# Optimization experiments

Hardware: AMD Instinct MI355X
Metric: run time of the kernel (lower is better)

The kernel has to match this reference:

```python
import jax, jax.numpy as jnp
import numpy as np

B = 16384        # batch
N_IN = 784       # n_input_neurons
D = 64           # n_neurons_per_hidd_bank
N_LAYERS = 6     # layers of hidden banks
BANKS = 6        # banks per layer (n_hidd_banks = 36)
N_OUT = 10       # n_output_neurons
EPS = 1e-5       # BatchNorm1d eps


def setup_inputs() -> dict:
    key = jax.random.key(0)
    ks = jax.random.split(key, 8)
    x = jax.random.normal(ks[0], (B, N_IN), dtype=jnp.float32)
    gamma_in = jnp.ones((N_IN,), jnp.float32)
    beta_in = jnp.zeros((N_IN,), jnp.float32)
    # input2hidden Linear(N_IN -> D) for each of the 6 input banks (layer 0)
    W_in = jax.random.normal(ks[1], (BANKS, D, N_IN), jnp.float32) * 0.03
    b_in = jax.random.normal(ks[2], (BANKS, D), jnp.float32) * 0.03
    # per-edge gate Linear(D -> 1, no bias) and data Linear(D -> D, bias)
    # indexed [layer, source_bank, target_bank, ...]
    Wg = jax.random.normal(ks[3], (N_LAYERS - 1, BANKS, BANKS, D), jnp.float32) * 0.1
    Wd = jax.random.normal(ks[4], (N_LAYERS - 1, BANKS, BANKS, D, D), jnp.float32) * 0.1
    bd = jax.random.normal(ks[5], (N_LAYERS - 1, BANKS, BANKS, D), jnp.float32) * 0.1
    # per-bank BatchNorm1d(D) affine params, [layer, bank, D]
    gamma_h = jnp.ones((N_LAYERS, BANKS, D), jnp.float32)
    beta_h = jnp.zeros((N_LAYERS, BANKS, D), jnp.float32)
    # hidden2output Linear(D -> N_OUT, no bias) for the 6 output banks (last layer)
    W_out = jax.random.normal(ks[6], (BANKS, N_OUT, D), jnp.float32) * 0.1
    return dict(x=x, gamma_in=gamma_in, beta_in=beta_in, W_in=W_in, b_in=b_in,
                Wg=Wg, Wd=Wd, bd=bd, gamma_h=gamma_h, beta_h=beta_h, W_out=W_out)


def _bn(x, g, b):
    # training-mode BatchNorm1d: normalize over batch axis 0, biased variance
    mu = jnp.mean(x, axis=0)
    var = jnp.mean((x - mu) ** 2, axis=0)
    return g * (x - mu) * jax.lax.rsqrt(var + EPS) + b


def reference(x, gamma_in, beta_in, W_in, b_in, Wg, Wd, bd, gamma_h, beta_h, W_out):
    xb = _bn(x, gamma_in, beta_in)                                  # [B, N_IN]
    # input banks: relu(input2hidden(x)); then (as targets with no sources)
    # relu (idempotent) + BatchNorm, matching the target loop in torch
    acts = jax.nn.relu(jnp.einsum('bn,kdn->bkd', xb, W_in) + b_in)  # [B, 6, D]
    acts = _bn(jax.nn.relu(acts), gamma_h[0], beta_h[0])
    total_gate = jnp.zeros((x.shape[0], 1), x.dtype)                # sum of [B,1] gate acts
    for l in range(N_LAYERS - 1):
        # gate: hardtanh(Linear(D->1), 0, 1) per edge (s,t)
        gate = jnp.clip(jnp.einsum('bsd,std->bst', acts, Wg[l]), 0.0, 1.0)  # [B,6,6]
        # data: Linear(D->D) per edge
        data = jnp.einsum('bsd,sted->bste', acts, Wd[l]) + bd[l]            # [B,6,6,D]
        pre = jnp.einsum('bst,bste->bte', gate, data)                       # sum over sources
        total_gate = total_gate + jnp.sum(gate, axis=(1, 2))[:, None]
        acts = _bn(jax.nn.relu(pre), gamma_h[l + 1], beta_h[l + 1])         # [B,6,D]
    # output banks = last layer banks; sum of Linear(D->N_OUT, no bias)
    output = jnp.einsum('bkd,kod->bo', acts, W_out)                         # [B, N_OUT]
    return output, total_gate
```

## Files before the change

### kernel.cpp

```cpp
#include <hip/hip_runtime.h>
#include <hip/hip_bf16.h>

#define BATCH   16384
#define NIN     784
#define NH      384
#define NLAYERS 6
#define NOUT    10
#define EPS_BN  1e-5f
#define LOSCALE 2048.0f
#define LOINV   (1.0f/2048.0f)
#define NPART   128
#define PSTRIDE 1024

typedef __attribute__((ext_vector_type(8))) _Float16 f16x8;
typedef __attribute__((ext_vector_type(4))) _Float16 f16x4;
typedef __attribute__((ext_vector_type(4))) float f32x4;

__global__ __launch_bounds__(256) void stats_partial(
        const float* __restrict__ src, int C, int applyRelu,
        float* __restrict__ psum, float* __restrict__ psq) {
    int c = blockIdx.x * 256 + threadIdx.x;
    if (c >= C) return;
    int r0 = blockIdx.y * (BATCH / NPART);
    float s = 0.f, q = 0.f;
    for (int r = r0; r < r0 + BATCH / NPART; ++r) {
        float v = src[(size_t)r * C + c];
        if (applyRelu) v = fmaxf(v, 0.f);
        s += v; q += v * v;
    }
    psum[blockIdx.y * PSTRIDE + c] = s;
    psq [blockIdx.y * PSTRIDE + c] = q;
}

__global__ __launch_bounds__(256) void stats_finalize(
        const float* __restrict__ psum, const float* __restrict__ psq, int C,
        const float* __restrict__ gamma, const float* __restrict__ beta,
        float* __restrict__ a_out, float* __restrict__ c_out) {
    int c = blockIdx.x * 256 + threadIdx.x;
    if (c >= C) return;
    float s = 0.f, q = 0.f;
    for (int i = 0; i < NPART; ++i) { s += psum[i * PSTRIDE + c]; q += psq[i * PSTRIDE + c]; }
    const float invB = 1.f / (float)BATCH;
    float mu  = s * invB;
    float var = q * invB - mu * mu;
    float rs  = rsqrtf(var + EPS_BN);
    float g   = gamma[c];
    a_out[c] = g * rs;
    c_out[c] = beta[c] - g * mu * rs;
}

__global__ __launch_bounds__(256) void scale_win_hl(
        const float* __restrict__ W_in, const float* __restrict__ a,
        _Float16* __restrict__ whi, _Float16* __restrict__ wlo) {
    int i = blockIdx.x * 256 + threadIdx.x;
    if (i >= NH * NIN / 4) return;
    int n = (i * 4) % NIN;
    float4 wv = ((const float4*)W_in)[i];
    float v[4] = { wv.x * a[n], wv.y * a[n + 1], wv.z * a[n + 2], wv.w * a[n + 3] };
    f16x4 h4, l4;
    #pragma unroll
    for (int j = 0; j < 4; ++j) {
        _Float16 h = (_Float16)v[j];
        h4[j] = h;
        l4[j] = (_Float16)((v[j] - (float)h) * LOSCALE);
    }
    *(f16x4*)(whi + (size_t)i * 4) = h4;
    *(f16x4*)(wlo + (size_t)i * 4) = l4;
}

__global__ __launch_bounds__(256) void conv_hl(
        const float* __restrict__ src, _Float16* __restrict__ hi,
        _Float16* __restrict__ lo, int n4) {
    int i = blockIdx.x * 256 + threadIdx.x;
    if (i >= n4) return;
    float4 wv = ((const float4*)src)[i];
    float v[4] = { wv.x, wv.y, wv.z, wv.w };
    f16x4 h4, l4;
    #pragma unroll
    for (int j = 0; j < 4; ++j) {
        _Float16 h = (_Float16)v[j];
        h4[j] = h;
        l4[j] = (_Float16)((v[j] - (float)h) * LOSCALE);
    }
    *(f16x4*)(hi + (size_t)i * 4) = h4;
    *(f16x4*)(lo + (size_t)i * 4) = l4;
}

__global__ __launch_bounds__(256) void prep_wg(
        const float* __restrict__ Wg, _Float16* __restrict__ hi,
        _Float16* __restrict__ lo) {
    int idx = blockIdx.x * 256 + threadIdx.x;
    if (idx >= 5 * 48 * 384) return;
    int l = idx / (48 * 384);
    int r = idx % (48 * 384);
    int st = r / 384, k = r % 384;
    float v = 0.f;
    if (st < 36 && (k >> 6) == st / 6)
        v = Wg[l * 36 * 64 + st * 64 + (k & 63)];
    _Float16 h = (_Float16)v;
    hi[idx] = h;
    lo[idx] = (_Float16)((v - (float)h) * LOSCALE);
}

__global__ __launch_bounds__(256) void prep_wout(
        const float* __restrict__ W_out, _Float16* __restrict__ hi,
        _Float16* __restrict__ lo) {
    int idx = blockIdx.x * 256 + threadIdx.x;
    if (idx >= 16 * 384) return;
    int o = idx / 384, k = idx % 384;
    float v = 0.f;
    if (o < NOUT) v = W_out[((k >> 6) * NOUT + o) * 64 + (k & 63)];
    _Float16 h = (_Float16)v;
    hi[idx] = h;
    lo[idx] = (_Float16)((v - (float)h) * LOSCALE);
}

__global__ __launch_bounds__(64) void bias_in(
        const float* __restrict__ W_in, const float* __restrict__ b_in,
        const float* __restrict__ cvec, float* __restrict__ bp) {
    int j = blockIdx.x;
    int lane = threadIdx.x;
    float s = 0.f;
    for (int n = lane; n < NIN; n += 64) s += cvec[n] * W_in[j * NIN + n];
    #pragma unroll
    for (int m = 1; m < 64; m <<= 1) s += __shfl_xor(s, m, 64);
    if (lane == 0) bp[j] = b_in[j] + s;
}

__global__ __launch_bounds__(256, 2) void gemm_in_mfma(
        const float* __restrict__ X, const _Float16* __restrict__ Wphi,
        const _Float16* __restrict__ Wplo, const float* __restrict__ bp,
        float* __restrict__ pre) {
    int tid = threadIdx.x;
    int w = tid >> 6, l = tid & 63, lr = l & 15, lq = l >> 4;
    int b0 = blockIdx.x * 128 + w * 32;
    int n0 = blockIdx.y * 96;
    const float* xrow0 = X + (size_t)(b0 + lr) * NIN;
    const float* xrow1 = X + (size_t)(b0 + 16 + lr) * NIN;
    f32x4 acc[6][2], acr[6][2];
    #pragma unroll
    for (int ct = 0; ct < 6; ++ct)
        #pragma unroll
        for (int bt = 0; bt < 2; ++bt)
            #pragma unroll
            for (int r = 0; r < 4; ++r) { acc[ct][bt][r] = 0.f; acr[ct][bt][r] = 0.f; }
    for (int kc = 0; kc < 24; ++kc) {
        int k0 = kc * 32 + lq * 8;
        f16x8 ahi[2], alo[2];
        {
            float4 x0 = *(const float4*)(xrow0 + k0);
            float4 x1 = *(const float4*)(xrow0 + k0 + 4);
            float xv[8] = { x0.x, x0.y, x0.z, x0.w, x1.x, x1.y, x1.z, x1.w };
            #pragma unroll
            for (int j = 0; j < 8; ++j) {
                _Float16 h = (_Float16)xv[j];
                ahi[0][j] = h;
                alo[0][j] = (_Float16)((xv[j] - (float)h) * LOSCALE);
            }
            float4 y0 = *(const float4*)(xrow1 + k0);
            float4 y1 = *(const float4*)(xrow1 + k0 + 4);
            float yv[8] = { y0.x, y0.y, y0.z, y0.w, y1.x, y1.y, y1.z, y1.w };
            #pragma unroll
            for (int j = 0; j < 8; ++j) {
                _Float16 h = (_Float16)yv[j];
                ahi[1][j] = h;
                alo[1][j] = (_Float16)((yv[j] - (float)h) * LOSCALE);
            }
        }
        #pragma unroll
        for (int ct = 0; ct < 6; ++ct) {
            size_t off = (size_t)(n0 + ct * 16 + lr) * NIN + k0;
            f16x8 bhi = *(const f16x8*)(Wphi + off);
            f16x8 blo = *(const f16x8*)(Wplo + off);
            #pragma unroll
            for (int bt = 0; bt < 2; ++bt) {
                acc[ct][bt] = __builtin_amdgcn_mfma_f32_16x16x32_f16(ahi[bt], bhi, acc[ct][bt], 0, 0, 0);
                acr[ct][bt] = __builtin_amdgcn_mfma_f32_16x16x32_f16(ahi[bt], blo, acr[ct][bt], 0, 0, 0);
                acr[ct][bt] = __builtin_amdgcn_mfma_f32_16x16x32_f16(alo[bt], bhi, acr[ct][bt], 0, 0, 0);
            }
        }
    }
    {
        f16x8 ahi[2], alo[2];
        #pragma unroll
        for (int bt = 0; bt < 2; ++bt)
            #pragma unroll
            for (int j = 0; j < 8; ++j) { ahi[bt][j] = (_Float16)0.f; alo[bt][j] = (_Float16)0.f; }
        if (lq < 2) {
            const float* xr[2] = { xrow0, xrow1 };
            #pragma unroll
            for (int bt = 0; bt < 2; ++bt) {
                float4 x0 = *(const float4*)(xr[bt] + 768 + lq * 8);
                float4 x1 = *(const float4*)(xr[bt] + 768 + lq * 8 + 4);
                float xv[8] = { x0.x, x0.y, x0.z, x0.w, x1.x, x1.y, x1.z, x1.w };
                #pragma unroll
                for (int j = 0; j < 8; ++j) {
                    _Float16 h = (_Float16)xv[j];
                    ahi[bt][j] = h;
                    alo[bt][j] = (_Float16)((xv[j] - (float)h) * LOSCALE);
                }
            }
        }
        #pragma unroll
        for (int ct = 0; ct < 6; ++ct) {
            f16x8 bhi, blo;
            #pragma unroll
            for (int j = 0; j < 8; ++j) { bhi[j] = (_Float16)0.f; blo[j] = (_Float16)0.f; }
            if (lq < 2) {
                size_t off = (size_t)(n0 + ct * 16 + lr) * NIN + 768 + lq * 8;
                bhi = *(const f16x8*)(Wphi + off);
                blo = *(const f16x8*)(Wplo + off);
            }
            #pragma unroll
            for (int bt = 0; bt < 2; ++bt) {
                acc[ct][bt] = __builtin_amdgcn_mfma_f32_16x16x32_f16(ahi[bt], bhi, acc[ct][bt], 0, 0, 0);
                acr[ct][bt] = __builtin_amdgcn_mfma_f32_16x16x32_f16(ahi[bt], blo, acr[ct][bt], 0, 0, 0);
                acr[ct][bt] = __builtin_amdgcn_mfma_f32_16x16x32_f16(alo[bt], bhi, acr[ct][bt], 0, 0, 0);
            }
        }
    }
    #pragma unroll
    for (int ct = 0; ct < 6; ++ct) {
        int n = n0 + ct * 16 + lr;
        float bias = bp[n];
        #pragma unroll
        for (int bt = 0; bt < 2; ++bt) {
            int brow = b0 + bt * 16 + lq * 4;
            #pragma unroll
            for (int r = 0; r < 4; ++r)
                pre[(size_t)(brow + r) * NH + n] = acc[ct][bt][r] + LOINV * acr[ct][bt][r] + bias;
        }
    }
}

__global__ __launch_bounds__(256) void norm_hl(
        const float* __restrict__ pre, const float* __restrict__ a,
        const float* __restrict__ c, _Float16* __restrict__ hi,
        _Float16* __restrict__ lo) {
    int idx = blockIdx.x * 256 + threadIdx.x;
    int j = (idx * 8) % NH;
    float4 v0 = ((const float4*)pre)[idx * 2];
    float4 v1 = ((const float4*)pre)[idx * 2 + 1];
    float y[8] = {
        a[j+0] * fmaxf(v0.x, 0.f) + c[j+0], a[j+1] * fmaxf(v0.y, 0.f) + c[j+1],
        a[j+2] * fmaxf(v0.z, 0.f) + c[j+2], a[j+3] * fmaxf(v0.w, 0.f) + c[j+3],
        a[j+4] * fmaxf(v1.x, 0.f) + c[j+4], a[j+5] * fmaxf(v1.y, 0.f) + c[j+5],
        a[j+6] * fmaxf(v1.z, 0.f) + c[j+6], a[j+7] * fmaxf(v1.w, 0.f) + c[j+7] };
    f16x8 h8, l8;
    #pragma unroll
    for (int jj = 0; jj < 8; ++jj) {
        _Float16 h = (_Float16)y[jj];
        h8[jj] = h;
        l8[jj] = (_Float16)((y[jj] - (float)h) * LOSCALE);
    }
    *(f16x8*)(hi + (size_t)idx * 8) = h8;
    *(f16x8*)(lo + (size_t)idx * 8) = l8;
}

__global__ __launch_bounds__(256, 2) void normgate_mfma(
        const float* __restrict__ pre, const float* __restrict__ a,
        const float* __restrict__ c, const _Float16* __restrict__ WgHi,
        const _Float16* __restrict__ WgLo, _Float16* __restrict__ aHi,
        _Float16* __restrict__ aLo, float* __restrict__ gateT,
        float* __restrict__ tg, int firstLayer) {
    int tid = threadIdx.x;
    int w = tid >> 6, l = tid & 63, lr = l & 15, lq = l >> 4;
    int b = blockIdx.x * 64 + w * 16 + lr;
    const float* prow = pre + (size_t)b * NH;
    f32x4 acc[3], acr[3];
    #pragma unroll
    for (int rt = 0; rt < 3; ++rt)
        #pragma unroll
        for (int r = 0; r < 4; ++r) { acc[rt][r] = 0.f; acr[rt][r] = 0.f; }
    #pragma unroll
    for (int kc = 0; kc < 12; ++kc) {
        int k0 = kc * 32 + lq * 8;
        float4 v0 = *(const float4*)(prow + k0);
        float4 v1 = *(const float4*)(prow + k0 + 4);
        float4 a0 = *(const float4*)(a + k0);
        float4 a1 = *(const float4*)(a + k0 + 4);
        float4 c0 = *(const float4*)(c + k0);
        float4 c1 = *(const float4*)(c + k0 + 4);
        float y[8] = {
            a0.x * fmaxf(v0.x, 0.f) + c0.x, a0.y * fmaxf(v0.y, 0.f) + c0.y,
            a0.z * fmaxf(v0.z, 0.f) + c0.z, a0.w * fmaxf(v0.w, 0.f) + c0.w,
            a1.x * fmaxf(v1.x, 0.f) + c1.x, a1.y * fmaxf(v1.y, 0.f) + c1.y,
            a1.z * fmaxf(v1.z, 0.f) + c1.z, a1.w * fmaxf(v1.w, 0.f) + c1.w };
        f16x8 bhi, blo;
        #pragma unroll
        for (int j = 0; j < 8; ++j) {
            _Float16 h = (_Float16)y[j];
            bhi[j] = h;
            blo[j] = (_Float16)((y[j] - (float)h) * LOSCALE);
        }
        *(f16x8*)(aHi + (size_t)b * NH + k0) = bhi;
        *(f16x8*)(aLo + (size_t)b * NH + k0) = blo;
        #pragma unroll
        for (int rt = 0; rt < 3; ++rt) {
            size_t off = (size_t)(rt * 16 + lr) * NH + k0;
            f16x8 whi = *(const f16x8*)(WgHi + off);
            f16x8 wlo = *(const f16x8*)(WgLo + off);
            acc[rt] = __builtin_amdgcn_mfma_f32_16x16x32_f16(whi, bhi, acc[rt], 0, 0, 0);
            acr[rt] = __builtin_amdgcn_mfma_f32_16x16x32_f16(whi, blo, acr[rt], 0, 0, 0);
            acr[rt] = __builtin_amdgcn_mfma_f32_16x16x32_f16(wlo, bhi, acr[rt], 0, 0, 0);
        }
    }
    float gsum = 0.f;
    #pragma unroll
    for (int rt = 0; rt < 3; ++rt)
        #pragma unroll
        for (int r = 0; r < 4; ++r) {
            int st = rt * 16 + lq * 4 + r;
            if (st < 36) {
                float p = acc[rt][r] + LOINV * acr[rt][r];
                float g = fminf(fmaxf(p, 0.f), 1.f);
                gateT[(size_t)st * BATCH + b] = g;
                gsum += g;
            }
        }
    gsum += __shfl_xor(gsum, 16, 64);
    gsum += __shfl_xor(gsum, 32, 64);
    if (lq == 0) tg[b] = (firstLayer ? 0.f : tg[b]) + gsum;
}

__global__ __launch_bounds__(256, 2) void layer_data_mfma(
        const _Float16* __restrict__ aHi, const _Float16* __restrict__ aLo,
        const float* __restrict__ gateT, const _Float16* __restrict__ Wdhi,
        const _Float16* __restrict__ Wdlo, const float* __restrict__ bd_l,
        float* __restrict__ pre) {
    int tid = threadIdx.x;
    int w = tid >> 6, l = tid & 63, lr = l & 15, lq = l >> 4;
    int b0 = blockIdx.x * 64;
    int t0 = blockIdx.y * 3;
    int e0 = w * 16;
    f32x4 acc[3][4];
    #pragma unroll
    for (int t = 0; t < 3; ++t)
        #pragma unroll
        for (int ct = 0; ct < 4; ++ct)
            #pragma unroll
            for (int r = 0; r < 4; ++r) acc[t][ct][r] = 0.f;
    for (int s = 0; s < 6; ++s) {
        f16x8 bhi[4][2], blo[4][2];
        #pragma unroll
        for (int ct = 0; ct < 4; ++ct) {
            size_t arow = (size_t)(b0 + ct * 16 + lr) * NH + s * 64 + lq * 8;
            #pragma unroll
            for (int ks = 0; ks < 2; ++ks) {
                bhi[ct][ks] = *(const f16x8*)(aHi + arow + ks * 32);
                blo[ct][ks] = *(const f16x8*)(aLo + arow + ks * 32);
            }
        }
        #pragma unroll
        for (int tt = 0; tt < 3; ++tt) {
            int t = t0 + tt;
            float g[4];
            #pragma unroll
            for (int ct = 0; ct < 4; ++ct)
                g[ct] = gateT[(size_t)(s * 6 + t) * BATCH + b0 + ct * 16 + lr];
            size_t wb = ((size_t)(s * 6 + t) * 64 + e0 + lr) * 64 + lq * 8;
            f16x8 ah0 = *(const f16x8*)(Wdhi + wb);
            f16x8 ah1 = *(const f16x8*)(Wdhi + wb + 32);
            f16x8 al0 = *(const f16x8*)(Wdlo + wb);
            f16x8 al1 = *(const f16x8*)(Wdlo + wb + 32);
            float bdv[4];
            #pragma unroll
            for (int r = 0; r < 4; ++r)
                bdv[r] = bd_l[(s * 6 + t) * 64 + e0 + lq * 4 + r];
            #pragma unroll
            for (int ct = 0; ct < 4; ++ct) {
                f32x4 ph, pc;
                #pragma unroll
                for (int r = 0; r < 4; ++r) { ph[r] = 0.f; pc[r] = 0.f; }
                ph = __builtin_amdgcn_mfma_f32_16x16x32_f16(ah0, bhi[ct][0], ph, 0, 0, 0);
                ph = __builtin_amdgcn_mfma_f32_16x16x32_f16(ah1, bhi[ct][1], ph, 0, 0, 0);
                pc = __builtin_amdgcn_mfma_f32_16x16x32_f16(ah0, blo[ct][0], pc, 0, 0, 0);
                pc = __builtin_amdgcn_mfma_f32_16x16x32_f16(ah1, blo[ct][1], pc, 0, 0, 0);
                pc = __builtin_amdgcn_mfma_f32_16x16x32_f16(al0, bhi[ct][0], pc, 0, 0, 0);
                pc = __builtin_amdgcn_mfma_f32_16x16x32_f16(al1, bhi[ct][1], pc, 0, 0, 0);
                #pragma unroll
                for (int r = 0; r < 4; ++r)
                    acc[tt][ct][r] += g[ct] * (ph[r] + LOINV * pc[r] + bdv[r]);
            }
        }
    }
    #pragma unroll
    for (int tt = 0; tt < 3; ++tt)
        #pragma unroll
        for (int ct = 0; ct < 4; ++ct)
            #pragma unroll
            for (int r = 0; r < 4; ++r)
                pre[(size_t)(b0 + ct * 16 + lr) * NH + (t0 + tt) * 64 + e0 + lq * 4 + r]
                    = acc[tt][ct][r];
}

__global__ __launch_bounds__(256, 2) void out_mfma(
        const _Float16* __restrict__ aHi, const _Float16* __restrict__ aLo,
        const _Float16* __restrict__ OutHi, const _Float16* __restrict__ OutLo,
        const float* __restrict__ tg, float* __restrict__ dout) {
    int tid = threadIdx.x;
    int w = tid >> 6, l = tid & 63, lr = l & 15, lq = l >> 4;
    int b = blockIdx.x * 64 + w * 16 + lr;
    const _Float16* arowH = aHi + (size_t)b * NH;
    const _Float16* arowL = aLo + (size_t)b * NH;
    f32x4 acc, acr;
    #pragma unroll
    for (int r = 0; r < 4; ++r) { acc[r] = 0.f; acr[r] = 0.f; }
    #pragma unroll
    for (int kc = 0; kc < 12; ++kc) {
        int k0 = kc * 32 + lq * 8;
        f16x8 bhi = *(const f16x8*)(arowH + k0);
        f16x8 blo = *(const f16x8*)(arowL + k0);
        size_t off = (size_t)lr * NH + k0;
        f16x8 ahi = *(const f16x8*)(OutHi + off);
        f16x8 alo = *(const f16x8*)(OutLo + off);
        acc = __builtin_amdgcn_mfma_f32_16x16x32_f16(ahi, bhi, acc, 0, 0, 0);
        acr = __builtin_amdgcn_mfma_f32_16x16x32_f16(ahi, blo, acr, 0, 0, 0);
        acr = __builtin_amdgcn_mfma_f32_16x16x32_f16(alo, bhi, acr, 0, 0, 0);
    }
    #pragma unroll
    for (int r = 0; r < 4; ++r) {
        int o = lq * 4 + r;
        if (o < NOUT)
            dout[(size_t)b * NOUT + o] = acc[r] + LOINV * acr[r];
    }
    if (lq == 0) dout[(size_t)BATCH * NOUT + b] = tg[b];
}

extern "C" void kernel_launch(void* const* d_in, const int* in_sizes, int n_in,
                              void* d_out, int out_size, void* d_ws, size_t ws_size,
                              hipStream_t stream) {
    const float* x        = (const float*)d_in[0];
    const float* gamma_in = (const float*)d_in[1];
    const float* beta_in  = (const float*)d_in[2];
    const float* W_in     = (const float*)d_in[3];
    const float* b_in     = (const float*)d_in[4];
    const float* Wg       = (const float*)d_in[5];
    const float* Wd       = (const float*)d_in[6];
    const float* bd       = (const float*)d_in[7];
    const float* gamma_h  = (const float*)d_in[8];
    const float* beta_h   = (const float*)d_in[9];
    const float* W_out    = (const float*)d_in[10];
    float* dout = (float*)d_out;
    float* ws = (float*)d_ws;

    float* psum  = ws;
    float* psq   = ws + 131072;
    float* avec  = ws + 262144;
    float* cvec  = ws + 263168;
    float* bp    = ws + 264192;
    float* pre   = ws + 265216;
    _Float16* actsHi = (_Float16*)(ws + 6556672);
    _Float16* actsLo = (_Float16*)(ws + 9702400);
    float* gateT = ws + 12848128;
    float* tg    = ws + 13437952;
    _Float16* WpHi = (_Float16*)(ws + 13454336);
    _Float16* WpLo = (_Float16*)(ws + 13604864);
    _Float16* WdHiAll = (_Float16*)(ws + 13755392);
    _Float16* WdLoAll = (_Float16*)(ws + 14124032);
    _Float16* WgHiAll = (_Float16*)(ws + 14492672);
    _Float16* WgLoAll = (_Float16*)(ws + 14538752);
    _Float16* OutHi   = (_Float16*)(ws + 14584832);
    _Float16* OutLo   = (_Float16*)(ws + 14587904);

    dim3 blk(256);

    stats_partial<<<dim3(4, NPART), blk, 0, stream>>>(x, NIN, 0, psum, psq);
    stats_finalize<<<dim3(4), blk, 0, stream>>>(psum, psq, NIN, gamma_in, beta_in, avec, cvec);
    scale_win_hl<<<dim3((NH * NIN / 4 + 255) / 256), blk, 0, stream>>>(W_in, avec, WpHi, WpLo);
    bias_in<<<dim3(NH), dim3(64), 0, stream>>>(W_in, b_in, cvec, bp);
    conv_hl<<<dim3((5 * 36 * 4096 / 4 + 255) / 256), blk, 0, stream>>>(
            Wd, WdHiAll, WdLoAll, 5 * 36 * 4096 / 4);
    prep_wg<<<dim3((5 * 48 * 384 + 255) / 256), blk, 0, stream>>>(Wg, WgHiAll, WgLoAll);
    prep_wout<<<dim3((16 * 384 + 255) / 256), blk, 0, stream>>>(W_out, OutHi, OutLo);

    gemm_in_mfma<<<dim3(BATCH / 128, 4), blk, 0, stream>>>(x, WpHi, WpLo, bp, pre);

    for (int j = 0; j < NLAYERS; ++j) {
        stats_partial<<<dim3(2, NPART), blk, 0, stream>>>(pre, NH, 1, psum, psq);
        stats_finalize<<<dim3(2), blk, 0, stream>>>(psum, psq, NH,
                gamma_h + j * NH, beta_h + j * NH, avec, cvec);
        if (j < NLAYERS - 1) {
            int l = j;
            normgate_mfma<<<dim3(BATCH / 64), blk, 0, stream>>>(
                    pre, avec, cvec, WgHiAll + (size_t)l * 48 * 384,
                    WgLoAll + (size_t)l * 48 * 384, actsHi, actsLo, gateT, tg, l == 0);
            layer_data_mfma<<<dim3(BATCH / 64, 2), blk, 0, stream>>>(
                    actsHi, actsLo, gateT, WdHiAll + (size_t)l * 36 * 4096,
                    WdLoAll + (size_t)l * 36 * 4096, bd + (size_t)l * 36 * 64, pre);
        } else {
            norm_hl<<<dim3(BATCH * NH / 8 / 256), blk, 0, stream>>>(
                    pre, avec, cvec, actsHi, actsLo);
        }
    }

    out_mfma<<<dim3(BATCH / 64), blk, 0, stream>>>(actsHi, actsLo, OutHi, OutLo, tg, dout);
}
```

Before: 607.7 us.

## Fuse final norm into output GEMM, split-K normgate, retile input GEMM

The final-layer norm_hl kernel and out_mfma are merged into normout_mfma, which normalizes pre on the fly and multiplies by W_out, so the hi/lo f16 activation buffers are no longer written and re-read. normgate_mfma and normout_mfma now split the K dimension across the four waves of a block, each handling 16 batch rows, and combine partial sums through shared memory. This gives four times as many blocks in exchange for a barrier and an LDS reduction. The input GEMM's column tile shrinks from 96 to 64 over a 6-wide grid, which cuts accumulator registers but reloads the X rows more often.

```diff
diff --git a/kernel.cpp b/kernel.cpp
--- a/kernel.cpp
+++ b/kernel.cpp
@@ -134,12 +134,12 @@
     int tid = threadIdx.x;
     int w = tid >> 6, l = tid & 63, lr = l & 15, lq = l >> 4;
     int b0 = blockIdx.x * 128 + w * 32;
-    int n0 = blockIdx.y * 96;
+    int n0 = blockIdx.y * 64;
     const float* xrow0 = X + (size_t)(b0 + lr) * NIN;
     const float* xrow1 = X + (size_t)(b0 + 16 + lr) * NIN;
-    f32x4 acc[6][2], acr[6][2];
-    #pragma unroll
-    for (int ct = 0; ct < 6; ++ct)
+    f32x4 acc[4][2], acr[4][2];
+    #pragma unroll
+    for (int ct = 0; ct < 4; ++ct)
         #pragma unroll
         for (int bt = 0; bt < 2; ++bt)
             #pragma unroll
@@ -168,7 +168,7 @@
             }
         }
         #pragma unroll
-        for (int ct = 0; ct < 6; ++ct) {
+        for (int ct = 0; ct < 4; ++ct) {
             size_t off = (size_t)(n0 + ct * 16 + lr) * NIN + k0;
             f16x8 bhi = *(const f16x8*)(Wphi + off);
             f16x8 blo = *(const f16x8*)(Wplo + off);
@@ -202,7 +202,7 @@
             }
         }
         #pragma unroll
-        for (int ct = 0; ct < 6; ++ct) {
+        for (int ct = 0; ct < 4; ++ct) {
             f16x8 bhi, blo;
             #pragma unroll
             for (int j = 0; j < 8; ++j) { bhi[j] = (_Float16)0.f; blo[j] = (_Float16)0.f; }
@@ -220,7 +220,7 @@
         }
     }
     #pragma unroll
-    for (int ct = 0; ct < 6; ++ct) {
+    for (int ct = 0; ct < 4; ++ct) {
         int n = n0 + ct * 16 + lr;
         float bias = bp[n];
         #pragma unroll
@@ -231,30 +231,6 @@
                 pre[(size_t)(brow + r) * NH + n] = acc[ct][bt][r] + LOINV * acr[ct][bt][r] + bias;
         }
     }
-}
-
-__global__ __launch_bounds__(256) void norm_hl(
-        const float* __restrict__ pre, const float* __restrict__ a,
-        const float* __restrict__ c, _Float16* __restrict__ hi,
-        _Float16* __restrict__ lo) {
-    int idx = blockIdx.x * 256 + threadIdx.x;
-    int j = (idx * 8) % NH;
-    float4 v0 = ((const float4*)pre)[idx * 2];
-    float4 v1 = ((const float4*)pre)[idx * 2 + 1];
-    float y[8] = {
-        a[j+0] * fmaxf(v0.x, 0.f) + c[j+0], a[j+1] * fmaxf(v0.y, 0.f) + c[j+1],
-        a[j+2] * fmaxf(v0.z, 0.f) + c[j+2], a[j+3] * fmaxf(v0.w, 0.f) + c[j+3],
-        a[j+4] * fmaxf(v1.x, 0.f) + c[j+4], a[j+5] * fmaxf(v1.y, 0.f) + c[j+5],
-        a[j+6] * fmaxf(v1.z, 0.f) + c[j+6], a[j+7] * fmaxf(v1.w, 0.f) + c[j+7] };
-    f16x8 h8, l8;
-    #pragma unroll
-    for (int jj = 0; jj < 8; ++jj) {
-        _Float16 h = (_Float16)y[jj];
-        h8[jj] = h;
-        l8[jj] = (_Float16)((y[jj] - (float)h) * LOSCALE);
-    }
-    *(f16x8*)(hi + (size_t)idx * 8) = h8;
-    *(f16x8*)(lo + (size_t)idx * 8) = l8;
 }
 
 __global__ __launch_bounds__(256, 2) void normgate_mfma(
@@ -263,9 +239,10 @@
         const _Float16* __restrict__ WgLo, _Float16* __restrict__ aHi,
         _Float16* __restrict__ aLo, float* __restrict__ gateT,
         float* __restrict__ tg, int firstLayer) {
+    __shared__ float red[24][3][64];
     int tid = threadIdx.x;
-    int w = tid >> 6, l = tid & 63, lr = l & 15, lq = l >> 4;
-    int b = blockIdx.x * 64 + w * 16 + lr;
+    int kw = tid >> 6, l = tid & 63, lr = l & 15, lq = l >> 4;
+    int b = blockIdx.x * 16 + lr;
     const float* prow = pre + (size_t)b * NH;
     f32x4 acc[3], acr[3];
     #pragma unroll
@@ -273,8 +250,8 @@
         #pragma unroll
         for (int r = 0; r < 4; ++r) { acc[rt][r] = 0.f; acr[rt][r] = 0.f; }
     #pragma unroll
-    for (int kc = 0; kc < 12; ++kc) {
-        int k0 = kc * 32 + lq * 8;
+    for (int kk = 0; kk < 3; ++kk) {
+        int k0 = (kw * 3 + kk) * 32 + lq * 8;
         float4 v0 = *(const float4*)(prow + k0);
         float4 v1 = *(const float4*)(prow + k0 + 4);
         float4 a0 = *(const float4*)(a + k0);
@@ -305,22 +282,44 @@
             acr[rt] = __builtin_amdgcn_mfma_f32_16x16x32_f16(wlo, bhi, acr[rt], 0, 0, 0);
         }
     }
-    float gsum = 0.f;
-    #pragma unroll
-    for (int rt = 0; rt < 3; ++rt)
-        #pragma unroll
-        for (int r = 0; r < 4; ++r) {
-            int st = rt * 16 + lq * 4 + r;
-            if (st < 36) {
-                float p = acc[rt][r] + LOINV * acr[rt][r];
-                float g = fminf(fmaxf(p, 0.f), 1.f);
-                gateT[(size_t)st * BATCH + b] = g;
-                gsum += g;
-            }
-        }
-    gsum += __shfl_xor(gsum, 16, 64);
-    gsum += __shfl_xor(gsum, 32, 64);
-    if (lq == 0) tg[b] = (firstLayer ? 0.f : tg[b]) + gsum;
+    if (kw > 0) {
+        #pragma unroll
+        for (int rt = 0; rt < 3; ++rt)
+            #pragma unroll
+            for (int r = 0; r < 4; ++r) {
+                red[rt * 4 + r][kw - 1][l]      = acc[rt][r];
+                red[12 + rt * 4 + r][kw - 1][l] = acr[rt][r];
+            }
+    }
+    __syncthreads();
+    if (kw == 0) {
+        #pragma unroll
+        for (int rt = 0; rt < 3; ++rt)
+            #pragma unroll
+            for (int r = 0; r < 4; ++r) {
+                #pragma unroll
+                for (int wv = 0; wv < 3; ++wv) {
+                    acc[rt][r] += red[rt * 4 + r][wv][l];
+                    acr[rt][r] += red[12 + rt * 4 + r][wv][l];
+                }
+            }
+        float gsum = 0.f;
+        #pragma unroll
+        for (int rt = 0; rt < 3; ++rt)
+            #pragma unroll
+            for (int r = 0; r < 4; ++r) {
+                int st = rt * 16 + lq * 4 + r;
+                if (st < 36) {
+                    float p = acc[rt][r] + LOINV * acr[rt][r];
+                    float g = fminf(fmaxf(p, 0.f), 1.f);
+                    gateT[(size_t)st * BATCH + b] = g;
+                    gsum += g;
+                }
+            }
+        gsum += __shfl_xor(gsum, 16, 64);
+        gsum += __shfl_xor(gsum, 32, 64);
+        if (lq == 0) tg[b] = (firstLayer ? 0.f : tg[b]) + gsum;
+    }
 }
 
 __global__ __launch_bounds__(256, 2) void layer_data_mfma(
@@ -394,37 +393,71 @@
                     = acc[tt][ct][r];
 }
 
-__global__ __launch_bounds__(256, 2) void out_mfma(
-        const _Float16* __restrict__ aHi, const _Float16* __restrict__ aLo,
-        const _Float16* __restrict__ OutHi, const _Float16* __restrict__ OutLo,
-        const float* __restrict__ tg, float* __restrict__ dout) {
+__global__ __launch_bounds__(256, 2) void normout_mfma(
+        const float* __restrict__ pre, const float* __restrict__ a,
+        const float* __restrict__ c, const _Float16* __restrict__ OutHi,
+        const _Float16* __restrict__ OutLo, const float* __restrict__ tg,
+        float* __restrict__ dout) {
+    __shared__ float red[8][3][64];
     int tid = threadIdx.x;
-    int w = tid >> 6, l = tid & 63, lr = l & 15, lq = l >> 4;
-    int b = blockIdx.x * 64 + w * 16 + lr;
-    const _Float16* arowH = aHi + (size_t)b * NH;
-    const _Float16* arowL = aLo + (size_t)b * NH;
+    int kw = tid >> 6, l = tid & 63, lr = l & 15, lq = l >> 4;
+    int b = blockIdx.x * 16 + lr;
+    const float* prow = pre + (size_t)b * NH;
     f32x4 acc, acr;
     #pragma unroll
     for (int r = 0; r < 4; ++r) { acc[r] = 0.f; acr[r] = 0.f; }
     #pragma unroll
-    for (int kc = 0; kc < 12; ++kc) {
-        int k0 = kc * 32 + lq * 8;
-        f16x8 bhi = *(const f16x8*)(arowH + k0);
-        f16x8 blo = *(const f16x8*)(arowL + k0);
+    for (int kk = 0; kk < 3; ++kk) {
+        int k0 = (kw * 3 + kk) * 32 + lq * 8;
+        float4 v0 = *(const float4*)(prow + k0);
+        float4 v1 = *(const float4*)(prow + k0 + 4);
+        float4 a0 = *(const float4*)(a + k0);
+        float4 a1 = *(const float4*)(a + k0 + 4);
+        float4 c0 = *(const float4*)(c + k0);
+        float4 c1 = *(const float4*)(c + k0 + 4);
+        float y[8] = {
+            a0.x * fmaxf(v0.x, 0.f) + c0.x, a0.y * fmaxf(v0.y, 0.f) + c0.y,
+            a0.z * fmaxf(v0.z, 0.f) + c0.z, a0.w * fmaxf(v0.w, 0.f) + c0.w,
+            a1.x * fmaxf(v1.x, 0.f) + c1.x, a1.y * fmaxf(v1.y, 0.f) + c1.y,
+            a1.z * fmaxf(v1.z, 0.f) + c1.z, a1.w * fmaxf(v1.w, 0.f) + c1.w };
+        f16x8 bhi, blo;
+        #pragma unroll
+        for (int j = 0; j < 8; ++j) {
+            _Float16 h = (_Float16)y[j];
+            bhi[j] = h;
+            blo[j] = (_Float16)((y[j] - (float)h) * LOSCALE);
+        }
         size_t off = (size_t)lr * NH + k0;
-        f16x8 ahi = *(const f16x8*)(OutHi + off);
-        f16x8 alo = *(const f16x8*)(OutLo + off);
-        acc = __builtin_amdgcn_mfma_f32_16x16x32_f16(ahi, bhi, acc, 0, 0, 0);
-        acr = __builtin_amdgcn_mfma_f32_16x16x32_f16(ahi, blo, acr, 0, 0, 0);
-        acr = __builtin_amdgcn_mfma_f32_16x16x32_f16(alo, bhi, acr, 0, 0, 0);
-    }
-    #pragma unroll
-    for (int r = 0; r < 4; ++r) {
-        int o = lq * 4 + r;
-        if (o < NOUT)
-            dout[(size_t)b * NOUT + o] = acc[r] + LOINV * acr[r];
-    }
-    if (lq == 0) dout[(size_t)BATCH * NOUT + b] = tg[b];
+        f16x8 whi = *(const f16x8*)(OutHi + off);
+        f16x8 wlo = *(const f16x8*)(OutLo + off);
+        acc = __builtin_amdgcn_mfma_f32_16x16x32_f16(whi, bhi, acc, 0, 0, 0);
+        acr = __builtin_amdgcn_mfma_f32_16x16x32_f16(whi, blo, acr, 0, 0, 0);
+        acr = __builtin_amdgcn_mfma_f32_16x16x32_f16(wlo, bhi, acr, 0, 0, 0);
+    }
+    if (kw > 0) {
+        #pragma unroll
+        for (int r = 0; r < 4; ++r) {
+            red[r][kw - 1][l]     = acc[r];
+            red[4 + r][kw - 1][l] = acr[r];
+        }
+    }
+    __syncthreads();
+    if (kw == 0) {
+        #pragma unroll
+        for (int r = 0; r < 4; ++r)
+            #pragma unroll
+            for (int wv = 0; wv < 3; ++wv) {
+                acc[r] += red[r][wv][l];
+                acr[r] += red[4 + r][wv][l];
+            }
+        #pragma unroll
+        for (int r = 0; r < 4; ++r) {
+            int o = lq * 4 + r;
+            if (o < NOUT)
+                dout[(size_t)b * NOUT + o] = acc[r] + LOINV * acr[r];
+        }
+        if (lq == 0) dout[(size_t)BATCH * NOUT + b] = tg[b];
+    }
 }
 
 extern "C" void kernel_launch(void* const* d_in, const int* in_sizes, int n_in,
@@ -474,7 +507,7 @@
     prep_wg<<<dim3((5 * 48 * 384 + 255) / 256), blk, 0, stream>>>(Wg, WgHiAll, WgLoAll);
     prep_wout<<<dim3((16 * 384 + 255) / 256), blk, 0, stream>>>(W_out, OutHi, OutLo);
 
-    gemm_in_mfma<<<dim3(BATCH / 128, 4), blk, 0, stream>>>(x, WpHi, WpLo, bp, pre);
+    gemm_in_mfma<<<dim3(BATCH / 128, 6), blk, 0, stream>>>(x, WpHi, WpLo, bp, pre);
 
     for (int j = 0; j < NLAYERS; ++j) {
         stats_partial<<<dim3(2, NPART), blk, 0, stream>>>(pre, NH, 1, psum, psq);
@@ -482,17 +515,15 @@
                 gamma_h + j * NH, beta_h + j * NH, avec, cvec);
         if (j < NLAYERS - 1) {
             int l = j;
-            normgate_mfma<<<dim3(BATCH / 64), blk, 0, stream>>>(
+            normgate_mfma<<<dim3(BATCH / 16), blk, 0, stream>>>(
                     pre, avec, cvec, WgHiAll + (size_t)l * 48 * 384,
                     WgLoAll + (size_t)l * 48 * 384, actsHi, actsLo, gateT, tg, l == 0);
             layer_data_mfma<<<dim3(BATCH / 64, 2), blk, 0, stream>>>(
                     actsHi, actsLo, gateT, WdHiAll + (size_t)l * 36 * 4096,
                     WdLoAll + (size_t)l * 36 * 4096, bd + (size_t)l * 36 * 64, pre);
         } else {
-            norm_hl<<<dim3(BATCH * NH / 8 / 256), blk, 0, stream>>>(
-                    pre, avec, cvec, actsHi, actsLo);
-        }
-    }
-
-    out_mfma<<<dim3(BATCH / 64), blk, 0, stream>>>(actsHi, actsLo, OutHi, OutLo, tg, dout);
-}
+            normout_mfma<<<dim3(BATCH / 16), blk, 0, stream>>>(
+                    pre, avec, cvec, OutHi, OutLo, tg, dout);
+        }
+    }
+}
```

New measurement: 571.8 us (median of 2 runs). 5.9% less time.
